# Kernel tuning notes

Hardware: AMD Instinct MI355X
Metric: run time of the kernel (lower is better)

The kernel has to match this reference:

```python
import jax, jax.numpy as jnp
import numpy as np

N_NODES = 100000
N_EDGES = 3200000
N_FEAT = 256
HIDDEN = 64
N_CLASSES = 6


def gcn_conv(x, W, b, src, dst, n_nodes):
    """PyG GCNConv: out = D^{-1/2} (A + I) D^{-1/2} X W + b (self-loops added)."""
    h = x @ W  # [N, out]
    loops = jnp.arange(n_nodes, dtype=src.dtype)
    src2 = jnp.concatenate([src, loops])
    dst2 = jnp.concatenate([dst, loops])
    # degree over destination nodes (edge weight 1), including self-loops
    deg = jax.ops.segment_sum(jnp.ones_like(dst2, dtype=h.dtype), dst2,
                              num_segments=n_nodes)
    dis = jnp.where(deg > 0, jax.lax.rsqrt(deg), 0.0)  # deg^{-1/2}
    norm = dis[src2] * dis[dst2]  # [E+N]
    msg = h[src2] * norm[:, None]  # gather + scale
    out = jax.ops.segment_sum(msg, dst2, num_segments=n_nodes)  # scatter-add
    return out + b


def setup_inputs() -> dict:
    key = jax.random.key(0)
    ks = jax.random.split(key, 5)
    x = jax.random.normal(ks[0], (N_NODES, N_FEAT), dtype=jnp.float32)
    edge_index = jax.random.randint(ks[1], (2, N_EDGES), 0, N_NODES, dtype=jnp.int64)
    W1 = jax.random.normal(ks[2], (N_FEAT, HIDDEN), dtype=jnp.float32) / np.sqrt(N_FEAT)
    b1 = jnp.zeros((HIDDEN,), dtype=jnp.float32)
    W2 = jax.random.normal(ks[3], (HIDDEN, HIDDEN), dtype=jnp.float32) / np.sqrt(HIDDEN)
    b2 = jnp.zeros((HIDDEN,), dtype=jnp.float32)
    Wfc = jax.random.normal(ks[4], (HIDDEN, N_CLASSES), dtype=jnp.float32) / np.sqrt(HIDDEN)
    bfc = jnp.zeros((N_CLASSES,), dtype=jnp.float32)
    return {"x": x, "edge_index": edge_index, "W1": W1, "b1": b1,
            "W2": W2, "b2": b2, "Wfc": Wfc, "bfc": bfc}


def reference(x, edge_index, W1, b1, W2, b2, Wfc, bfc):
    src, dst = edge_index[0], edge_index[1]
    n = x.shape[0]
    h = jax.nn.relu(gcn_conv(x, W1, b1, src, dst, n))
    # dropout(p=0.2) is identity in eval mode
    h = jax.nn.relu(gcn_conv(h, W2, b2, src, dst, n))
    return h @ Wfc + bfc
```

## Files before the change

kernel.cpp:

```cpp
#include <hip/hip_runtime.h>
#include <hip/hip_fp16.h>
#include <math.h>

#define NFEAT 256
#define HID 64
#define NCLS 6
#define NBMX 1600
#define CAPB 4096
#define CHUNK 16384
#define XPAD 68
#define FUSED_LDS ((4096 + 64 * XPAD) * 4)

typedef float vf4 __attribute__((ext_vector_type(4)));
typedef int   vi4 __attribute__((ext_vector_type(4)));


__global__ __launch_bounds__(256) void k_count(const int* __restrict__ dst,
                                               int* __restrict__ C, int E, int nbuck) {
  __shared__ int cnt[NBMX];
  int t = threadIdx.x;
  for (int i = t; i < nbuck; i += 256) cnt[i] = 0;
  __syncthreads();
  int e0 = blockIdx.x * CHUNK;
  int e1 = e0 + CHUNK;
  if (e1 > E) e1 = E;
  for (int r0 = e0; r0 < e1; r0 += 1024) {
    int i0 = r0 + t * 4;
    if (i0 + 4 <= e1) {
      vi4 dv = __builtin_nontemporal_load((const vi4*)&dst[i0]);
      atomicAdd(&cnt[dv.x >> 6], 1);
      atomicAdd(&cnt[dv.y >> 6], 1);
      atomicAdd(&cnt[dv.z >> 6], 1);
      atomicAdd(&cnt[dv.w >> 6], 1);
    } else {
      for (int q = 0; q < 4; ++q)
        if (i0 + q < e1) atomicAdd(&cnt[dst[i0 + q] >> 6], 1);
    }
  }
  __syncthreads();
  int* Crow = C + (size_t)blockIdx.x * nbuck;
  for (int i = t; i < nbuck; i += 256) Crow[i] = cnt[i];
}


__global__ __launch_bounds__(256) void k_scan_cols(int* __restrict__ C,
                                                   int* __restrict__ T,
                                                   int nblk, int nbuck) {
  int b = blockIdx.x * 256 + threadIdx.x;
  if (b >= nbuck) return;
  int run = 0;
  int blk = 0;
  for (; blk + 4 <= nblk; blk += 4) {
    int c0 = C[(size_t)(blk + 0) * nbuck + b];
    int c1 = C[(size_t)(blk + 1) * nbuck + b];
    int c2 = C[(size_t)(blk + 2) * nbuck + b];
    int c3 = C[(size_t)(blk + 3) * nbuck + b];
    C[(size_t)(blk + 0) * nbuck + b] = run; run += c0;
    C[(size_t)(blk + 1) * nbuck + b] = run; run += c1;
    C[(size_t)(blk + 2) * nbuck + b] = run; run += c2;
    C[(size_t)(blk + 3) * nbuck + b] = run; run += c3;
  }
  for (; blk < nblk; ++blk) {
    int c = C[(size_t)blk * nbuck + b];
    C[(size_t)blk * nbuck + b] = run;
    run += c;
  }
  T[b] = run;
}


__global__ __launch_bounds__(256) void k_scanb(const int* __restrict__ T,
                                               int* __restrict__ bbase, int nbuck) {
  __shared__ int sh[256];
  __shared__ int carry;
  int t = threadIdx.x;
  if (t == 0) carry = 0;
  __syncthreads();
  for (int base = 0; base < nbuck; base += 256) {
    int v = (base + t < nbuck) ? T[base + t] : 0;
    sh[t] = v;
    __syncthreads();
    for (int off = 1; off < 256; off <<= 1) {
      int x = sh[t];
      int y = (t >= off) ? sh[t - off] : 0;
      __syncthreads();
      sh[t] = x + y;
      __syncthreads();
    }
    if (base + t < nbuck) bbase[base + t] = carry + sh[t] - v;
    __syncthreads();
    if (t == 255) carry += sh[255];
    __syncthreads();
  }
}


__global__ __launch_bounds__(256) void k_fused(const int* __restrict__ src,
                                               const int* __restrict__ dst,
                                               const int* __restrict__ C,
                                               const int* __restrict__ bbase,
                                               unsigned* __restrict__ packed,
                                               int E, int nbuck, int nbb,
                                               const float* __restrict__ X,
                                               const float* __restrict__ W1,
                                               __half* __restrict__ H16, int n) {
  extern __shared__ char smem[];
  int t = threadIdx.x;

  if (blockIdx.x < nbb) {
    int* baseL = (int*)smem;
    int* cnt   = baseL + NBMX;
    const int* Crow = C + (size_t)blockIdx.x * nbuck;
    for (int i = t; i < nbuck; i += 256) {
      baseL[i] = bbase[i] + Crow[i];
      cnt[i] = 0;
    }
    __syncthreads();

    int e0 = blockIdx.x * CHUNK;
    int e1 = e0 + CHUNK;
    if (e1 > E) e1 = E;
    for (int r0 = e0; r0 < e1; r0 += 1024) {
      int i0 = r0 + t * 4;
      int s4[4], d4[4];
      bool full = (i0 + 4 <= e1);
      if (full) {
        vi4 sv = __builtin_nontemporal_load((const vi4*)&src[i0]);
        vi4 dv = __builtin_nontemporal_load((const vi4*)&dst[i0]);
        s4[0] = sv.x; s4[1] = sv.y; s4[2] = sv.z; s4[3] = sv.w;
        d4[0] = dv.x; d4[1] = dv.y; d4[2] = dv.z; d4[3] = dv.w;
      } else {
        for (int q = 0; q < 4; ++q)
          if (i0 + q < e1) { s4[q] = src[i0 + q]; d4[q] = dst[i0 + q]; }
      }
#pragma unroll
      for (int q = 0; q < 4; ++q) {
        if (i0 + q < e1) {
          int b = d4[q] >> 6;
          int slot = atomicAdd(&cnt[b], 1);
          packed[(size_t)baseL[b] + slot] =
              ((unsigned)s4[q] << 6) | (unsigned)(d4[q] & 63);
        }
      }
    }
  } else {
    float* Wl = (float*)smem;
    float* Xl = Wl + 4096;
    const int row0 = (blockIdx.x - nbb) * 64;
    const int tc = t & 15;
    const int tr = t >> 4;
    float acc[4][4] = {};

    for (int k0 = 0; k0 < NFEAT; k0 += 64) {
      __syncthreads();
#pragma unroll
      for (int i = 0; i < 4; ++i) {
        int idx = t * 4 + i * 1024;
        int kr = idx >> 6, c = idx & 63;
        *(vf4*)&Wl[idx] = *(const vf4*)&W1[(size_t)(k0 + kr) * 64 + c];
      }
#pragma unroll
      for (int i = 0; i < 4; ++i) {
        int idx = t * 4 + i * 1024;
        int r = idx >> 6, c = idx & 63;
        int row = row0 + r;
        vf4 v = {0.f, 0.f, 0.f, 0.f};
        if (row < n) v = __builtin_nontemporal_load((const vf4*)&X[(size_t)row * NFEAT + k0 + c]);
        *(vf4*)&Xl[r * XPAD + c] = v;
      }
      __syncthreads();
#pragma unroll 4
      for (int kk = 0; kk < 64; kk += 4) {
        float4 xv[4], wv[4];
#pragma unroll
        for (int r = 0; r < 4; ++r) xv[r] = *(float4*)&Xl[(tr * 4 + r) * XPAD + kk];
#pragma unroll
        for (int q = 0; q < 4; ++q) wv[q] = *(float4*)&Wl[(kk + q) * 64 + tc * 4];
#pragma unroll
        for (int r = 0; r < 4; ++r) {
          const float xr[4] = {xv[r].x, xv[r].y, xv[r].z, xv[r].w};
#pragma unroll
          for (int q = 0; q < 4; ++q) {
            acc[r][0] += xr[q] * wv[q].x;
            acc[r][1] += xr[q] * wv[q].y;
            acc[r][2] += xr[q] * wv[q].z;
            acc[r][3] += xr[q] * wv[q].w;
          }
        }
      }
    }
#pragma unroll
    for (int r = 0; r < 4; ++r) {
      int row = row0 + tr * 4 + r;
      if (row < n) {
        __half2 h01 = __floats2half2_rn(acc[r][0], acc[r][1]);
        __half2 h23 = __floats2half2_rn(acc[r][2], acc[r][3]);
        uint2 st;
        st.x = *reinterpret_cast<unsigned*>(&h01);
        st.y = *reinterpret_cast<unsigned*>(&h23);
        ((uint2*)H16)[(size_t)row * 16 + tc] = st;
      }
    }
  }
}


__global__ __launch_bounds__(256) void k_build(unsigned* __restrict__ packed,
                                               const int* __restrict__ T,
                                               const int* __restrict__ bbase,
                                               int2* __restrict__ rowrange,
                                               float* __restrict__ dis,
                                               __half* __restrict__ g1,
                                               int n, int nbuck) {
  __shared__ unsigned buf[CAPB];
  __shared__ unsigned outb[CAPB];
  __shared__ int cnt4[4][64];
  __shared__ int cur4[4][64];
  __shared__ int offi[64];
  __shared__ int offx[64];
  __shared__ int cntl[64];
  __shared__ float disl[64];
  int b = blockIdx.x;
  int t = threadIdx.x;
  int g = t >> 6;
  int m = T[b];
  if (m > CAPB) m = CAPB;
  int bb = bbase[b];
  unsigned* pb = packed + bb;

  cnt4[g][t & 63] = 0;
  for (int k = t; k < m; k += 256) buf[k] = pb[k];
  __syncthreads();
  for (int k = t; k < m; k += 256) atomicAdd(&cnt4[g][buf[k] & 63u], 1);
  __syncthreads();
  if (t < 64) {
    int c0 = cnt4[0][t], c1 = cnt4[1][t], c2 = cnt4[2][t], c3 = cnt4[3][t];
    int tot = c0 + c1 + c2 + c3;
    cntl[t] = tot;
    offi[t] = tot;
    cur4[0][t] = 0;
    cur4[1][t] = c0;
    cur4[2][t] = c0 + c1;
    cur4[3][t] = c0 + c1 + c2;
  }
  __syncthreads();
  for (int off = 1; off < 64; off <<= 1) {
    int x = (t < 64) ? offi[t] : 0;
    int y = (t >= off && t < 64) ? offi[t - off] : 0;
    __syncthreads();
    if (t < 64) offi[t] = x + y;
    __syncthreads();
  }
  if (t < 64) {
    offx[t] = offi[t] - cntl[t];
    float dv = rsqrtf((float)cntl[t] + 1.0f);
    disl[t] = dv;
    int v = b * 64 + t;
    if (v < n) {
      rowrange[v] = make_int2(bb + offx[t], cntl[t]);
      dis[v] = dv;
    }
#pragma unroll
    for (int gg = 0; gg < 4; ++gg) cur4[gg][t] += offx[t];
  }
  __syncthreads();
  for (int k = t; k < m; k += 256) {
    unsigned e = buf[k];
    int dl = e & 63u;
    int q = atomicAdd(&cur4[g][dl], 1);
    outb[q] = e >> 6;
  }
  __syncthreads();
  for (int k = t; k < m; k += 256) pb[k] = outb[k];

  __half2* g1h = (__half2*)g1;
#pragma unroll
  for (int i = 0; i < 8; ++i) {
    int idx = t + i * 256;
    int r = idx >> 5, e = idx & 31;
    int v = b * 64 + r;
    if (v < n) {
      size_t p = (size_t)v * 32 + e;
      float2 f = __half22float2(g1h[p]);
      float d = disl[r];
      g1h[p] = __floats2half2_rn(f.x * d, f.y * d);
    }
  }
}


__global__ __launch_bounds__(256) void k_agg_gemm(const int2* __restrict__ rowrange,
                                                  const int* __restrict__ srcs,
                                                  const __half* __restrict__ g16,
                                                  const float* __restrict__ dis,
                                                  const float* __restrict__ b1,
                                                  const float* __restrict__ W2,
                                                  __half* __restrict__ g2out, int n) {
  __shared__ __half2 W2h[64 * 32];
  int t = threadIdx.x;
  for (int i = t; i < 2048; i += 256) {
    float2 f = *(const float2*)&W2[(size_t)i * 2];
    W2h[i] = __floats2half2_rn(f.x, f.y);
  }
  __syncthreads();

  int grp = t >> 4, lane = t & 15;
  int v = blockIdx.x * 16 + grp;
  if (v >= n) return;
  const uint2* g2 = (const uint2*)g16;

  int2 rr = rowrange[v];
  int j = rr.x, end = rr.x + rr.y;
  uint2 su = g2[(size_t)v * 16 + lane];
  float2 f0 = __half22float2(*reinterpret_cast<__half2*>(&su.x));
  float2 f1 = __half22float2(*reinterpret_cast<__half2*>(&su.y));
  float ax = f0.x, ay = f0.y, az = f1.x, aw = f1.y;

  for (; j + 8 <= end; j += 8) {
    int s[8];
#pragma unroll
    for (int q = 0; q < 8; ++q) s[q] = __builtin_nontemporal_load(&srcs[j + q]);
    uint2 a[8];
#pragma unroll
    for (int q = 0; q < 8; ++q) a[q] = g2[(size_t)s[q] * 16 + lane];
#pragma unroll
    for (int q = 0; q < 8; ++q) {
      float2 p0 = __half22float2(*reinterpret_cast<__half2*>(&a[q].x));
      float2 p1 = __half22float2(*reinterpret_cast<__half2*>(&a[q].y));
      ax += p0.x; ay += p0.y; az += p1.x; aw += p1.y;
    }
  }
  for (; j < end; ++j) {
    int s0 = __builtin_nontemporal_load(&srcs[j]);
    uint2 a0 = g2[(size_t)s0 * 16 + lane];
    float2 p0 = __half22float2(*reinterpret_cast<__half2*>(&a0.x));
    float2 p1 = __half22float2(*reinterpret_cast<__half2*>(&a0.y));
    ax += p0.x; ay += p0.y; az += p1.x; aw += p1.y;
  }

  float dv = dis[v];
  float4 bb = *(const float4*)&b1[lane * 4];
  float r0 = fmaxf(fmaf(dv, ax, bb.x), 0.f);
  float r1 = fmaxf(fmaf(dv, ay, bb.y), 0.f);
  float r2 = fmaxf(fmaf(dv, az, bb.z), 0.f);
  float r3 = fmaxf(fmaf(dv, aw, bb.w), 0.f);

  float o0 = 0.f, o1 = 0.f, o2 = 0.f, o3 = 0.f;
  int gbase = (t & 63) & 48;
  int c2 = lane * 2;
#pragma unroll
  for (int kk = 0; kk < 16; ++kk) {
    int sl = gbase + kk;
    float a0 = __shfl(r0, sl, 64);
    float a1 = __shfl(r1, sl, 64);
    float a2 = __shfl(r2, sl, 64);
    float a3 = __shfl(r3, sl, 64);
    int k = kk * 4;
    float2 w;
    w = __half22float2(W2h[(k + 0) * 32 + c2]);     o0 = fmaf(a0, w.x, o0); o1 = fmaf(a0, w.y, o1);
    w = __half22float2(W2h[(k + 0) * 32 + c2 + 1]); o2 = fmaf(a0, w.x, o2); o3 = fmaf(a0, w.y, o3);
    w = __half22float2(W2h[(k + 1) * 32 + c2]);     o0 = fmaf(a1, w.x, o0); o1 = fmaf(a1, w.y, o1);
    w = __half22float2(W2h[(k + 1) * 32 + c2 + 1]); o2 = fmaf(a1, w.x, o2); o3 = fmaf(a1, w.y, o3);
    w = __half22float2(W2h[(k + 2) * 32 + c2]);     o0 = fmaf(a2, w.x, o0); o1 = fmaf(a2, w.y, o1);
    w = __half22float2(W2h[(k + 2) * 32 + c2 + 1]); o2 = fmaf(a2, w.x, o2); o3 = fmaf(a2, w.y, o3);
    w = __half22float2(W2h[(k + 3) * 32 + c2]);     o0 = fmaf(a3, w.x, o0); o1 = fmaf(a3, w.y, o1);
    w = __half22float2(W2h[(k + 3) * 32 + c2 + 1]); o2 = fmaf(a3, w.x, o2); o3 = fmaf(a3, w.y, o3);
  }
  __half2 h01 = __floats2half2_rn(o0 * dv, o1 * dv);
  __half2 h23 = __floats2half2_rn(o2 * dv, o3 * dv);
  uint2 st;
  st.x = *reinterpret_cast<unsigned*>(&h01);
  st.y = *reinterpret_cast<unsigned*>(&h23);
  ((uint2*)g2out)[(size_t)v * 16 + lane] = st;
}


__global__ __launch_bounds__(256) void k_agg_fc(const int2* __restrict__ rowrange,
                                                const int* __restrict__ srcs,
                                                const __half* __restrict__ g16,
                                                const float* __restrict__ dis,
                                                const float* __restrict__ b2,
                                                const float* __restrict__ Wfc,
                                                const float* __restrict__ bfc,
                                                float* __restrict__ outp, int n) {
  __shared__ float Wl[64 * NCLS];
  __shared__ float bl[8];
  int t = threadIdx.x;
  for (int i = t; i < 64 * NCLS; i += 256) Wl[i] = Wfc[i];
  if (t < NCLS) bl[t] = bfc[t];
  __syncthreads();

  int grp = t >> 4, lane = t & 15;
  int v = blockIdx.x * 16 + grp;
  bool active = (v < n);
  const uint2* g2 = (const uint2*)g16;

  float r0 = 0.f, r1 = 0.f, r2 = 0.f, r3 = 0.f;
  if (active) {
    int2 rr = rowrange[v];
    int j = rr.x, end = rr.x + rr.y;
    uint2 su = g2[(size_t)v * 16 + lane];
    float2 f0 = __half22float2(*reinterpret_cast<__half2*>(&su.x));
    float2 f1 = __half22float2(*reinterpret_cast<__half2*>(&su.y));
    float ax = f0.x, ay = f0.y, az = f1.x, aw = f1.y;

    for (; j + 8 <= end; j += 8) {
      int s[8];
#pragma unroll
      for (int q = 0; q < 8; ++q) s[q] = __builtin_nontemporal_load(&srcs[j + q]);
      uint2 a[8];
#pragma unroll
      for (int q = 0; q < 8; ++q) a[q] = g2[(size_t)s[q] * 16 + lane];
#pragma unroll
      for (int q = 0; q < 8; ++q) {
        float2 p0 = __half22float2(*reinterpret_cast<__half2*>(&a[q].x));
        float2 p1 = __half22float2(*reinterpret_cast<__half2*>(&a[q].y));
        ax += p0.x; ay += p0.y; az += p1.x; aw += p1.y;
      }
    }
    for (; j < end; ++j) {
      int s0 = __builtin_nontemporal_load(&srcs[j]);
      uint2 a0 = g2[(size_t)s0 * 16 + lane];
      float2 p0 = __half22float2(*reinterpret_cast<__half2*>(&a0.x));
      float2 p1 = __half22float2(*reinterpret_cast<__half2*>(&a0.y));
      ax += p0.x; ay += p0.y; az += p1.x; aw += p1.y;
    }
    float dv = dis[v];
    float4 bb = *(const float4*)&b2[lane * 4];
    r0 = fmaxf(fmaf(dv, ax, bb.x), 0.f);
    r1 = fmaxf(fmaf(dv, ay, bb.y), 0.f);
    r2 = fmaxf(fmaf(dv, az, bb.z), 0.f);
    r3 = fmaxf(fmaf(dv, aw, bb.w), 0.f);
  }

  float p[NCLS];
#pragma unroll
  for (int jj = 0; jj < NCLS; ++jj) p[jj] = 0.f;
  int k0 = lane * 4;
#pragma unroll
  for (int q = 0; q < 4; ++q) {
    float a = (q == 0) ? r0 : (q == 1) ? r1 : (q == 2) ? r2 : r3;
#pragma unroll
    for (int jj = 0; jj < NCLS; ++jj)
      p[jj] = fmaf(a, Wl[(k0 + q) * NCLS + jj], p[jj]);
  }
#pragma unroll
  for (int m = 1; m < 16; m <<= 1) {
#pragma unroll
    for (int jj = 0; jj < NCLS; ++jj)
      p[jj] += __shfl_xor(p[jj], m, 64);
  }
  if (active && lane < NCLS)
    outp[(size_t)v * NCLS + lane] = p[lane] + bl[lane];
}


extern "C" void kernel_launch(void* const* d_in, const int* in_sizes, int n_in,
                              void* d_out, int out_size, void* d_ws, size_t ws_size,
                              hipStream_t stream) {
  const float* x   = (const float*)d_in[0];
  const int*   ei  = (const int*)d_in[1];
  const float* W1  = (const float*)d_in[2];
  const float* b1  = (const float*)d_in[3];
  const float* W2  = (const float*)d_in[4];
  const float* b2  = (const float*)d_in[5];
  const float* Wfc = (const float*)d_in[6];
  const float* bfc = (const float*)d_in[7];
  float* out = (float*)d_out;

  const int n = in_sizes[0] / NFEAT;
  const int E = in_sizes[1] / 2;
  const int* src = ei;
  const int* dst = ei + E;
  const int nbuck = (n + 63) >> 6;
  const int nbb = (E + CHUNK - 1) / CHUNK;
  const int ntile = (n + 63) / 64;

  char* ws = (char*)d_ws;
  size_t off = 0;
  auto alloc = [&](size_t bytes) -> void* {
    void* p = (void*)(ws + off);
    off += (bytes + 255) & ~(size_t)255;
    return p;
  };
  float* dis      = (float*)alloc((size_t)n * 4);
  int2*  rowrange = (int2*)alloc((size_t)n * 8);
  int*   C        = (int*)alloc((size_t)nbb * nbuck * 4);
  int*   T        = (int*)alloc((size_t)nbuck * 4);
  int*   bbase    = (int*)alloc((size_t)nbuck * 4);
  unsigned* packed = (unsigned*)alloc((size_t)E * 4);
  __half* bufA16  = (__half*)alloc((size_t)n * HID * 2);
  __half* bufC16  = (__half*)alloc((size_t)n * HID * 2);

  k_count<<<nbb, 256, 0, stream>>>(dst, C, E, nbuck);
  k_scan_cols<<<(nbuck + 255) / 256, 256, 0, stream>>>(C, T, nbb, nbuck);
  k_scanb<<<1, 256, 0, stream>>>(T, bbase, nbuck);
  k_fused<<<nbb + ntile, 256, FUSED_LDS, stream>>>(src, dst, C, bbase, packed,
                                                   E, nbuck, nbb, x, W1, bufA16, n);
  k_build<<<nbuck, 256, 0, stream>>>(packed, T, bbase, rowrange, dis, bufA16, n, nbuck);

  k_agg_gemm<<<(n + 15) / 16, 256, 0, stream>>>(rowrange, (const int*)packed, bufA16,
                                                dis, b1, W2, bufC16, n);

  k_agg_fc<<<(n + 15) / 16, 256, 0, stream>>>(rowrange, (const int*)packed, bufC16,
                                              dis, b2, Wfc, bfc, out, n);
}
```

Baseline: 285.3 us.

## Scatter edges into block-local bucket segments and gather per bucket in build

The partition step now writes each edge into a bucket-sorted segment inside its own chunk's region, using a per-block local scan stored in L, instead of scattering it straight to the global bucket position. k_build then gathers each bucket's pieces from every chunk (one thread per chunk, serial copy) and writes the sorted sources to a separate srcs array. The aim is to make the scatter writes local and contiguous within each chunk's region rather than spread across the whole edge array. The cost is an extra scan in k_fused, an extra buffer and a serial, poorly coalesced per-thread gather loop in k_build.

```diff
diff --git a/kernel.cpp b/kernel.cpp
--- a/kernel.cpp
+++ b/kernel.cpp
@@ -98,26 +98,61 @@
 __global__ __launch_bounds__(256) void k_fused(const int* __restrict__ src,
                                                const int* __restrict__ dst,
                                                const int* __restrict__ C,
-                                               const int* __restrict__ bbase,
+                                               const int* __restrict__ T,
+                                               int* __restrict__ L,
                                                unsigned* __restrict__ packed,
                                                int E, int nbuck, int nbb,
                                                const float* __restrict__ X,
                                                const float* __restrict__ W1,
                                                __half* __restrict__ H16, int n) {
   extern __shared__ char smem[];
+  __shared__ int tsum[256];
   int t = threadIdx.x;
 
   if (blockIdx.x < nbb) {
     int* baseL = (int*)smem;
     int* cnt   = baseL + NBMX;
-    const int* Crow = C + (size_t)blockIdx.x * nbuck;
-    for (int i = t; i < nbuck; i += 256) {
-      baseL[i] = bbase[i] + Crow[i];
-      cnt[i] = 0;
-    }
-    __syncthreads();
-
-    int e0 = blockIdx.x * CHUNK;
+    const int blk = blockIdx.x;
+    const int* Crow = C + (size_t)blk * nbuck;
+    bool last = (blk == nbb - 1);
+    const int* CrowN = C + (size_t)(blk + 1) * nbuck;
+    int* Lrow = L + (size_t)blk * nbuck;
+
+    for (int b = t; b < nbuck; b += 256)
+      baseL[b] = (last ? T[b] : CrowN[b]) - Crow[b];
+    __syncthreads();
+    int base0 = t * 7;
+    int c7[7];
+    int s = 0;
+#pragma unroll
+    for (int i = 0; i < 7; ++i) {
+      int b = base0 + i;
+      c7[i] = (b < nbuck) ? baseL[b] : 0;
+      s += c7[i];
+    }
+    tsum[t] = s;
+    __syncthreads();
+    for (int off = 1; off < 256; off <<= 1) {
+      int x = tsum[t];
+      int y = (t >= off) ? tsum[t - off] : 0;
+      __syncthreads();
+      tsum[t] = x + y;
+      __syncthreads();
+    }
+    int run = tsum[t] - s;
+#pragma unroll
+    for (int i = 0; i < 7; ++i) {
+      int b = base0 + i;
+      if (b < nbuck) {
+        Lrow[b] = run;
+        baseL[b] = blk * CHUNK + run;
+        cnt[b] = 0;
+      }
+      run += c7[i];
+    }
+    __syncthreads();
+
+    int e0 = blk * CHUNK;
     int e1 = e0 + CHUNK;
     if (e1 > E) e1 = E;
     for (int r0 = e0; r0 < e1; r0 += 1024) {
@@ -205,13 +240,16 @@
 }
 
 
-__global__ __launch_bounds__(256) void k_build(unsigned* __restrict__ packed,
+__global__ __launch_bounds__(256) void k_build(const unsigned* __restrict__ packed,
+                                               const int* __restrict__ C,
+                                               const int* __restrict__ L,
                                                const int* __restrict__ T,
                                                const int* __restrict__ bbase,
+                                               int* __restrict__ srcs,
                                                int2* __restrict__ rowrange,
                                                float* __restrict__ dis,
                                                __half* __restrict__ g1,
-                                               int n, int nbuck) {
+                                               int n, int nbuck, int nbb) {
   __shared__ unsigned buf[CAPB];
   __shared__ unsigned outb[CAPB];
   __shared__ int cnt4[4][64];
@@ -226,10 +264,17 @@
   int m = T[b];
   if (m > CAPB) m = CAPB;
   int bb = bbase[b];
-  unsigned* pb = packed + bb;
 
   cnt4[g][t & 63] = 0;
-  for (int k = t; k < m; k += 256) buf[k] = pb[k];
+  if (t < nbb) {
+    int P = C[(size_t)t * nbuck + b];
+    int Pe = (t == nbb - 1) ? T[b] : C[(size_t)(t + 1) * nbuck + b];
+    if (Pe > CAPB) Pe = CAPB;
+    if (P < Pe) {
+      const unsigned* sp = packed + (size_t)t * CHUNK + L[(size_t)t * nbuck + b];
+      for (int k = 0; k < Pe - P; ++k) buf[P + k] = sp[k];
+    }
+  }
   __syncthreads();
   for (int k = t; k < m; k += 256) atomicAdd(&cnt4[g][buf[k] & 63u], 1);
   __syncthreads();
@@ -271,7 +316,7 @@
     outb[q] = e >> 6;
   }
   __syncthreads();
-  for (int k = t; k < m; k += 256) pb[k] = outb[k];
+  for (int k = t; k < m; k += 256) srcs[bb + k] = (int)outb[k];
 
   __half2* g1h = (__half2*)g1;
 #pragma unroll
@@ -486,22 +531,25 @@
   float* dis      = (float*)alloc((size_t)n * 4);
   int2*  rowrange = (int2*)alloc((size_t)n * 8);
   int*   C        = (int*)alloc((size_t)nbb * nbuck * 4);
+  int*   L        = (int*)alloc((size_t)nbb * nbuck * 4);
   int*   T        = (int*)alloc((size_t)nbuck * 4);
   int*   bbase    = (int*)alloc((size_t)nbuck * 4);
-  unsigned* packed = (unsigned*)alloc((size_t)E * 4);
+  unsigned* packed = (unsigned*)alloc((size_t)nbb * CHUNK * 4);
+  int*   srcs     = (int*)alloc((size_t)E * 4);
   __half* bufA16  = (__half*)alloc((size_t)n * HID * 2);
   __half* bufC16  = (__half*)alloc((size_t)n * HID * 2);
 
   k_count<<<nbb, 256, 0, stream>>>(dst, C, E, nbuck);
   k_scan_cols<<<(nbuck + 255) / 256, 256, 0, stream>>>(C, T, nbb, nbuck);
   k_scanb<<<1, 256, 0, stream>>>(T, bbase, nbuck);
-  k_fused<<<nbb + ntile, 256, FUSED_LDS, stream>>>(src, dst, C, bbase, packed,
+  k_fused<<<nbb + ntile, 256, FUSED_LDS, stream>>>(src, dst, C, T, L, packed,
                                                    E, nbuck, nbb, x, W1, bufA16, n);
-  k_build<<<nbuck, 256, 0, stream>>>(packed, T, bbase, rowrange, dis, bufA16, n, nbuck);
-
-  k_agg_gemm<<<(n + 15) / 16, 256, 0, stream>>>(rowrange, (const int*)packed, bufA16,
+  k_build<<<nbuck, 256, 0, stream>>>(packed, C, L, T, bbase, srcs, rowrange, dis,
+                                     bufA16, n, nbuck, nbb);
+
+  k_agg_gemm<<<(n + 15) / 16, 256, 0, stream>>>(rowrange, srcs, bufA16,
                                                 dis, b1, W2, bufC16, n);
 
-  k_agg_fc<<<(n + 15) / 16, 256, 0, stream>>>(rowrange, (const int*)packed, bufC16,
+  k_agg_fc<<<(n + 15) / 16, 256, 0, stream>>>(rowrange, srcs, bufC16,
                                               dis, b2, Wfc, bfc, out, n);
 }
```

New measurement: 292.8 us. 2.6% more time.

## Spread first-layer GEMM tiles across count, scan and scatter kernels

Applied to the files above, without the earlier changes.

The X·W1 GEMM tiles, which previously all ran inside the scatter kernel, are now split across three launches. Some tiles go to the count kernel, some to the column-scan kernel, and the rest to the scatter kernel, so the small, under-occupied count and scan launches get useful parallel work. The edge chunk size is also halved, which doubles the number of count and scatter blocks and the size of the per-block count matrix. The cost is larger LDS allocations for the count and scan blocks, and a longer serial column scan over twice as many rows.

```diff
diff --git a/kernel.cpp b/kernel.cpp
--- a/kernel.cpp
+++ b/kernel.cpp
@@ -7,65 +7,148 @@
 #define NCLS 6
 #define NBMX 1600
 #define CAPB 4096
-#define CHUNK 16384
+#define CHUNK 8192
 #define XPAD 68
 #define FUSED_LDS ((4096 + 64 * XPAD) * 4)
+#define TILES_CNT 280
+#define TILES_SCN 320
 
 typedef float vf4 __attribute__((ext_vector_type(4)));
 typedef int   vi4 __attribute__((ext_vector_type(4)));
 
 
-__global__ __launch_bounds__(256) void k_count(const int* __restrict__ dst,
-                                               int* __restrict__ C, int E, int nbuck) {
-  __shared__ int cnt[NBMX];
-  int t = threadIdx.x;
-  for (int i = t; i < nbuck; i += 256) cnt[i] = 0;
-  __syncthreads();
-  int e0 = blockIdx.x * CHUNK;
-  int e1 = e0 + CHUNK;
-  if (e1 > E) e1 = E;
-  for (int r0 = e0; r0 < e1; r0 += 1024) {
-    int i0 = r0 + t * 4;
-    if (i0 + 4 <= e1) {
-      vi4 dv = __builtin_nontemporal_load((const vi4*)&dst[i0]);
-      atomicAdd(&cnt[dv.x >> 6], 1);
-      atomicAdd(&cnt[dv.y >> 6], 1);
-      atomicAdd(&cnt[dv.z >> 6], 1);
-      atomicAdd(&cnt[dv.w >> 6], 1);
-    } else {
-      for (int q = 0; q < 4; ++q)
-        if (i0 + q < e1) atomicAdd(&cnt[dst[i0 + q] >> 6], 1);
-    }
-  }
-  __syncthreads();
-  int* Crow = C + (size_t)blockIdx.x * nbuck;
-  for (int i = t; i < nbuck; i += 256) Crow[i] = cnt[i];
-}
-
-
-__global__ __launch_bounds__(256) void k_scan_cols(int* __restrict__ C,
-                                                   int* __restrict__ T,
-                                                   int nblk, int nbuck) {
-  int b = blockIdx.x * 256 + threadIdx.x;
-  if (b >= nbuck) return;
-  int run = 0;
-  int blk = 0;
-  for (; blk + 4 <= nblk; blk += 4) {
-    int c0 = C[(size_t)(blk + 0) * nbuck + b];
-    int c1 = C[(size_t)(blk + 1) * nbuck + b];
-    int c2 = C[(size_t)(blk + 2) * nbuck + b];
-    int c3 = C[(size_t)(blk + 3) * nbuck + b];
-    C[(size_t)(blk + 0) * nbuck + b] = run; run += c0;
-    C[(size_t)(blk + 1) * nbuck + b] = run; run += c1;
-    C[(size_t)(blk + 2) * nbuck + b] = run; run += c2;
-    C[(size_t)(blk + 3) * nbuck + b] = run; run += c3;
-  }
-  for (; blk < nblk; ++blk) {
-    int c = C[(size_t)blk * nbuck + b];
-    C[(size_t)blk * nbuck + b] = run;
-    run += c;
-  }
-  T[b] = run;
+__device__ __forceinline__ void gemm1_tile(char* smem, int tile, int t,
+                                           const float* __restrict__ X,
+                                           const float* __restrict__ W1,
+                                           __half* __restrict__ H16, int n) {
+  float* Wl = (float*)smem;
+  float* Xl = Wl + 4096;
+  const int row0 = tile * 64;
+  const int tc = t & 15;
+  const int tr = t >> 4;
+  float acc[4][4] = {};
+
+  for (int k0 = 0; k0 < NFEAT; k0 += 64) {
+    __syncthreads();
+#pragma unroll
+    for (int i = 0; i < 4; ++i) {
+      int idx = t * 4 + i * 1024;
+      int kr = idx >> 6, c = idx & 63;
+      *(vf4*)&Wl[idx] = *(const vf4*)&W1[(size_t)(k0 + kr) * 64 + c];
+    }
+#pragma unroll
+    for (int i = 0; i < 4; ++i) {
+      int idx = t * 4 + i * 1024;
+      int r = idx >> 6, c = idx & 63;
+      int row = row0 + r;
+      vf4 v = {0.f, 0.f, 0.f, 0.f};
+      if (row < n) v = __builtin_nontemporal_load((const vf4*)&X[(size_t)row * NFEAT + k0 + c]);
+      *(vf4*)&Xl[r * XPAD + c] = v;
+    }
+    __syncthreads();
+#pragma unroll 4
+    for (int kk = 0; kk < 64; kk += 4) {
+      float4 xv[4], wv[4];
+#pragma unroll
+      for (int r = 0; r < 4; ++r) xv[r] = *(float4*)&Xl[(tr * 4 + r) * XPAD + kk];
+#pragma unroll
+      for (int q = 0; q < 4; ++q) wv[q] = *(float4*)&Wl[(kk + q) * 64 + tc * 4];
+#pragma unroll
+      for (int r = 0; r < 4; ++r) {
+        const float xr[4] = {xv[r].x, xv[r].y, xv[r].z, xv[r].w};
+#pragma unroll
+        for (int q = 0; q < 4; ++q) {
+          acc[r][0] += xr[q] * wv[q].x;
+          acc[r][1] += xr[q] * wv[q].y;
+          acc[r][2] += xr[q] * wv[q].z;
+          acc[r][3] += xr[q] * wv[q].w;
+        }
+      }
+    }
+  }
+#pragma unroll
+  for (int r = 0; r < 4; ++r) {
+    int row = row0 + tr * 4 + r;
+    if (row < n) {
+      __half2 h01 = __floats2half2_rn(acc[r][0], acc[r][1]);
+      __half2 h23 = __floats2half2_rn(acc[r][2], acc[r][3]);
+      uint2 st;
+      st.x = *reinterpret_cast<unsigned*>(&h01);
+      st.y = *reinterpret_cast<unsigned*>(&h23);
+      ((uint2*)H16)[(size_t)row * 16 + tc] = st;
+    }
+  }
+}
+
+
+__global__ __launch_bounds__(256) void k_count_f(const int* __restrict__ dst,
+                                                 int* __restrict__ C, int E, int nbuck, int nbb,
+                                                 const float* __restrict__ X,
+                                                 const float* __restrict__ W1,
+                                                 __half* __restrict__ H16, int n) {
+  extern __shared__ char smem[];
+  int t = threadIdx.x;
+  if (blockIdx.x < nbb) {
+    int* cnt = (int*)smem;
+    for (int i = t; i < nbuck; i += 256) cnt[i] = 0;
+    __syncthreads();
+    int e0 = blockIdx.x * CHUNK;
+    int e1 = e0 + CHUNK;
+    if (e1 > E) e1 = E;
+    for (int r0 = e0; r0 < e1; r0 += 1024) {
+      int i0 = r0 + t * 4;
+      if (i0 + 4 <= e1) {
+        vi4 dv = __builtin_nontemporal_load((const vi4*)&dst[i0]);
+        atomicAdd(&cnt[dv.x >> 6], 1);
+        atomicAdd(&cnt[dv.y >> 6], 1);
+        atomicAdd(&cnt[dv.z >> 6], 1);
+        atomicAdd(&cnt[dv.w >> 6], 1);
+      } else {
+        for (int q = 0; q < 4; ++q)
+          if (i0 + q < e1) atomicAdd(&cnt[dst[i0 + q] >> 6], 1);
+      }
+    }
+    __syncthreads();
+    int* Crow = C + (size_t)blockIdx.x * nbuck;
+    for (int i = t; i < nbuck; i += 256) Crow[i] = cnt[i];
+  } else {
+    gemm1_tile(smem, (int)blockIdx.x - nbb, t, X, W1, H16, n);
+  }
+}
+
+
+__global__ __launch_bounds__(256) void k_scan_f(int* __restrict__ C,
+                                                int* __restrict__ T,
+                                                int nblk, int nbuck, int nsb,
+                                                const float* __restrict__ X,
+                                                const float* __restrict__ W1,
+                                                __half* __restrict__ H16, int n, int tile0) {
+  extern __shared__ char smem[];
+  int t = threadIdx.x;
+  if (blockIdx.x < (unsigned)nsb) {
+    int b = blockIdx.x * 256 + t;
+    if (b >= nbuck) return;
+    int run = 0;
+    int blk = 0;
+    for (; blk + 4 <= nblk; blk += 4) {
+      int c0 = C[(size_t)(blk + 0) * nbuck + b];
+      int c1 = C[(size_t)(blk + 1) * nbuck + b];
+      int c2 = C[(size_t)(blk + 2) * nbuck + b];
+      int c3 = C[(size_t)(blk + 3) * nbuck + b];
+      C[(size_t)(blk + 0) * nbuck + b] = run; run += c0;
+      C[(size_t)(blk + 1) * nbuck + b] = run; run += c1;
+      C[(size_t)(blk + 2) * nbuck + b] = run; run += c2;
+      C[(size_t)(blk + 3) * nbuck + b] = run; run += c3;
+    }
+    for (; blk < nblk; ++blk) {
+      int c = C[(size_t)blk * nbuck + b];
+      C[(size_t)blk * nbuck + b] = run;
+      run += c;
+    }
+    T[b] = run;
+  } else {
+    gemm1_tile(smem, tile0 + (int)blockIdx.x - nsb, t, X, W1, H16, n);
+  }
 }
 
 
@@ -103,7 +186,7 @@
                                                int E, int nbuck, int nbb,
                                                const float* __restrict__ X,
                                                const float* __restrict__ W1,
-                                               __half* __restrict__ H16, int n) {
+                                               __half* __restrict__ H16, int n, int tile0) {
   extern __shared__ char smem[];
   int t = threadIdx.x;
 
@@ -144,63 +227,7 @@
       }
     }
   } else {
-    float* Wl = (float*)smem;
-    float* Xl = Wl + 4096;
-    const int row0 = (blockIdx.x - nbb) * 64;
-    const int tc = t & 15;
-    const int tr = t >> 4;
-    float acc[4][4] = {};
-
-    for (int k0 = 0; k0 < NFEAT; k0 += 64) {
-      __syncthreads();
-#pragma unroll
-      for (int i = 0; i < 4; ++i) {
-        int idx = t * 4 + i * 1024;
-        int kr = idx >> 6, c = idx & 63;
-        *(vf4*)&Wl[idx] = *(const vf4*)&W1[(size_t)(k0 + kr) * 64 + c];
-      }
-#pragma unroll
-      for (int i = 0; i < 4; ++i) {
-        int idx = t * 4 + i * 1024;
-        int r = idx >> 6, c = idx & 63;
-        int row = row0 + r;
-        vf4 v = {0.f, 0.f, 0.f, 0.f};
-        if (row < n) v = __builtin_nontemporal_load((const vf4*)&X[(size_t)row * NFEAT + k0 + c]);
-        *(vf4*)&Xl[r * XPAD + c] = v;
-      }
-      __syncthreads();
-#pragma unroll 4
-      for (int kk = 0; kk < 64; kk += 4) {
-        float4 xv[4], wv[4];
-#pragma unroll
-        for (int r = 0; r < 4; ++r) xv[r] = *(float4*)&Xl[(tr * 4 + r) * XPAD + kk];
-#pragma unroll
-        for (int q = 0; q < 4; ++q) wv[q] = *(float4*)&Wl[(kk + q) * 64 + tc * 4];
-#pragma unroll
-        for (int r = 0; r < 4; ++r) {
-          const float xr[4] = {xv[r].x, xv[r].y, xv[r].z, xv[r].w};
-#pragma unroll
-          for (int q = 0; q < 4; ++q) {
-            acc[r][0] += xr[q] * wv[q].x;
-            acc[r][1] += xr[q] * wv[q].y;
-            acc[r][2] += xr[q] * wv[q].z;
-            acc[r][3] += xr[q] * wv[q].w;
-          }
-        }
-      }
-    }
-#pragma unroll
-    for (int r = 0; r < 4; ++r) {
-      int row = row0 + tr * 4 + r;
-      if (row < n) {
-        __half2 h01 = __floats2half2_rn(acc[r][0], acc[r][1]);
-        __half2 h23 = __floats2half2_rn(acc[r][2], acc[r][3]);
-        uint2 st;
-        st.x = *reinterpret_cast<unsigned*>(&h01);
-        st.y = *reinterpret_cast<unsigned*>(&h23);
-        ((uint2*)H16)[(size_t)row * 16 + tc] = st;
-      }
-    }
+    gemm1_tile(smem, tile0 + (int)blockIdx.x - nbb, t, X, W1, H16, n);
   }
 }
 
@@ -475,6 +502,11 @@
   const int nbuck = (n + 63) >> 6;
   const int nbb = (E + CHUNK - 1) / CHUNK;
   const int ntile = (n + 63) / 64;
+  const int nsb = (nbuck + 255) / 256;
+  int tc = TILES_CNT, ts = TILES_SCN;
+  if (tc > ntile) tc = ntile;
+  if (tc + ts > ntile) ts = ntile - tc;
+  const int tf = ntile - tc - ts;
 
   char* ws = (char*)d_ws;
   size_t off = 0;
@@ -492,11 +524,11 @@
   __half* bufA16  = (__half*)alloc((size_t)n * HID * 2);
   __half* bufC16  = (__half*)alloc((size_t)n * HID * 2);
 
-  k_count<<<nbb, 256, 0, stream>>>(dst, C, E, nbuck);
-  k_scan_cols<<<(nbuck + 255) / 256, 256, 0, stream>>>(C, T, nbb, nbuck);
+  k_count_f<<<nbb + tc, 256, FUSED_LDS, stream>>>(dst, C, E, nbuck, nbb, x, W1, bufA16, n);
+  k_scan_f<<<nsb + ts, 256, FUSED_LDS, stream>>>(C, T, nbb, nbuck, nsb, x, W1, bufA16, n, tc);
   k_scanb<<<1, 256, 0, stream>>>(T, bbase, nbuck);
-  k_fused<<<nbb + ntile, 256, FUSED_LDS, stream>>>(src, dst, C, bbase, packed,
-                                                   E, nbuck, nbb, x, W1, bufA16, n);
+  k_fused<<<nbb + tf, 256, FUSED_LDS, stream>>>(src, dst, C, bbase, packed,
+                                                E, nbuck, nbb, x, W1, bufA16, n, tc + ts);
   k_build<<<nbuck, 256, 0, stream>>>(packed, T, bbase, rowrange, dis, bufA16, n, nbuck);
 
   k_agg_gemm<<<(n + 15) / 16, 256, 0, stream>>>(rowrange, (const int*)packed, bufA16,
```

After: 315.3 us. 1.11x slower.
